# Performance work log

Measured on AMD Instinct MI355X. Metric: run time of the kernel, lower is better.

The kernel has to match this reference:

```python
import jax, jax.numpy as jnp
import numpy as np

CROP_H, CROP_W = 7, 7

def _sample_coords(lo, hi, extent, n):
    # TF crop_and_resize: coord = lo*(extent-1) + i*(hi-lo)*(extent-1)/(n-1)
    step = (hi - lo) * (extent - 1) / (n - 1)          # [N]
    return lo[:, None] * (extent - 1) + jnp.arange(n, dtype=lo.dtype)[None, :] * step[:, None]  # [N, n]

def crop_and_resize(image, boxes, box_ind, crop_h, crop_w):
    # image: [B,H,W,C], boxes: [N,4] normalized (y1,x1,y2,x2), box_ind: [N]
    B, H, W, C = image.shape
    y1, x1, y2, x2 = boxes[:, 0], boxes[:, 1], boxes[:, 2], boxes[:, 3]
    ys = _sample_coords(y1, y2, H, crop_h)             # [N, crop_h]
    xs = _sample_coords(x1, x2, W, crop_w)             # [N, crop_w]

    y0 = jnp.floor(ys); x0 = jnp.floor(xs)
    wy = (ys - y0)[:, :, None, None]                    # [N,ch,1,1] lerp weight
    wx = (xs - x0)[:, None, :, None]                    # [N,1,cw,1]
    y0i = jnp.clip(y0.astype(jnp.int32), 0, H - 1)
    y1i = jnp.clip(y0i + 1, 0, H - 1)
    x0i = jnp.clip(x0.astype(jnp.int32), 0, W - 1)
    x1i = jnp.clip(x0i + 1, 0, W - 1)

    b = box_ind[:, None, None]                          # [N,1,1]
    def corner(yi, xi):                                 # -> [N,ch,cw,C]
        return image[b, yi[:, :, None], xi[:, None, :]]

    top = corner(y0i, x0i) + (corner(y0i, x1i) - corner(y0i, x0i)) * wx
    bot = corner(y1i, x0i) + (corner(y1i, x1i) - corner(y1i, x0i)) * wx
    out = top + (bot - top) * wy                        # [N,ch,cw,C]

    # TF uses extrapolation_value=0 for samples outside the image
    vy = ((ys >= 0) & (ys <= H - 1))[:, :, None, None]
    vx = ((xs >= 0) & (xs <= W - 1))[:, None, :, None]
    return jnp.where(vy & vx, out, jnp.zeros((), out.dtype))


def setup_inputs() -> dict:
    key = jax.random.key(0)
    k1, k2, k3 = jax.random.split(key, 3)
    feats = jax.random.normal(k1, (8, 64, 64, 256), dtype=jnp.float32)
    boxes = jax.random.uniform(k2, (4000, 4), dtype=jnp.float32)
    box_ind = jax.random.randint(k3, (4000, 1), 0, 8, dtype=jnp.int32)
    return {"feats": feats, "boxes": boxes, "box_ind": box_ind}


def reference(feats, boxes, box_ind):
    ind = box_ind.reshape(-1)
    return crop_and_resize(feats, boxes, ind, CROP_H, CROP_W)
```

## Files before the change

### kernel.cpp

```cpp
#include <hip/hip_runtime.h>


#define H 64
#define W 64
#define C 256
#define CROP_HW 49
#define NIMG 8
#define G 8

typedef float f32x4 __attribute__((ext_vector_type(4)));

__global__ __launch_bounds__(512) void bucket_kernel(
    const int* __restrict__ box_ind,
    int* __restrict__ order,
    int* __restrict__ offsets,
    int n)
{
    const int wave = threadIdx.x >> 6;
    const int lane = threadIdx.x & 63;
    __shared__ int counts[NIMG];

    int cnt = 0;
    for (int i = lane; i < n; i += 64)
        cnt += (box_ind[i] == wave);
    for (int off = 32; off; off >>= 1)
        cnt += __shfl_down(cnt, off);
    if (lane == 0) counts[wave] = cnt;
    __syncthreads();

    int start = 0;
    for (int i = 0; i < wave; ++i) start += counts[i];
    if (threadIdx.x == 0) {
        int acc = 0;
        for (int i = 0; i < NIMG; ++i) { offsets[i] = acc; acc += counts[i]; }
        offsets[NIMG] = acc;
    }

    int pos = start;
    for (int base = 0; base < n; base += 64) {
        const int i = base + lane;
        const bool m = (i < n) && (box_ind[i] == wave);
        const unsigned long long mask = __ballot(m);
        const int below = __popcll(mask & ((1ULL << lane) - 1ULL));
        if (m) order[pos + below] = i;
        pos += __popcll(mask);
    }
}

struct Cell {
    int p00, p01, p10, p11;
    float wx, wy;
    bool valid;
    int oidx;
};

__device__ __forceinline__ Cell cell_info(
    int c, const int* __restrict__ order, const f32x4* __restrict__ boxes4,
    int start)
{
    Cell k;
    const int bi = c / CROP_HW;
    const int r  = c - bi * CROP_HW;
    const int iy = r / 7;
    const int ix = r - iy * 7;
    const int b  = order[start + bi];

    const f32x4 bx = boxes4[b];

    const float stepy = (bx.z - bx.x) * 63.0f / 6.0f;
    const float stepx = (bx.w - bx.y) * 63.0f / 6.0f;
    const float ys = bx.x * 63.0f + (float)iy * stepy;
    const float xs = bx.y * 63.0f + (float)ix * stepx;

    const float y0f = floorf(ys);
    const float x0f = floorf(xs);
    k.wy = ys - y0f;
    k.wx = xs - x0f;

    const int y0 = min(max((int)y0f, 0), H - 1);
    const int y1 = min(y0 + 1, H - 1);
    const int x0 = min(max((int)x0f, 0), W - 1);
    const int x1 = min(x0 + 1, W - 1);

    k.valid = (ys >= 0.0f) && (ys <= (float)(H - 1)) &&
              (xs >= 0.0f) && (xs <= (float)(W - 1));

    k.p00 = y0 * W + x0;
    k.p01 = y0 * W + x1;
    k.p10 = y1 * W + x0;
    k.p11 = y1 * W + x1;

    k.oidx = (b * CROP_HW + r) * (C / 4);
    return k;
}

__global__ __launch_bounds__(256) void crop_resize_xcd(
    const float* __restrict__ feats,
    const float* __restrict__ boxes,
    const int*   __restrict__ order,
    const int*   __restrict__ offsets,
    float*       __restrict__ out)
{
    const int img  = blockIdx.x & 7;
    const int slot = blockIdx.x >> 3;
    const int lane = threadIdx.x & 63;
    const int wv   = threadIdx.x >> 6;

    const int start   = offsets[img];
    const int nb      = offsets[img + 1] - start;
    const int ncells  = nb * CROP_HW;
    const int ngroups = (ncells + G - 1) / G;
    const int wave_local = slot * 4 + wv;
    const int stride     = (gridDim.x >> 3) * 4;

    const f32x4* __restrict__ f4 = reinterpret_cast<const f32x4*>(feats)
                                   + (size_t)img * (H * W * (C / 4));
    const f32x4* __restrict__ boxes4 = reinterpret_cast<const f32x4*>(boxes);
    f32x4* __restrict__ o4 = reinterpret_cast<f32x4*>(out);

    for (int gi = wave_local; gi < ngroups; gi += stride) {
        const int cbase = gi * G;
        const int nval  = min(G, ncells - cbase);

        int c = cbase + (lane & (G - 1));
        if (c > ncells - 1) c = ncells - 1;
        const Cell k = cell_info(c, order, boxes4, start);
        const unsigned long long vmask = __ballot(k.valid);

        #pragma unroll
        for (int j = 0; j < G; ++j) {
            if (j >= nval) break;
            const int   s00 = __builtin_amdgcn_readlane(k.p00, j);
            const int   s01 = __builtin_amdgcn_readlane(k.p01, j);
            const int   s10 = __builtin_amdgcn_readlane(k.p10, j);
            const int   s11 = __builtin_amdgcn_readlane(k.p11, j);
            const float swx = __uint_as_float(
                __builtin_amdgcn_readlane(__float_as_uint(k.wx), j));
            const float swy = __uint_as_float(
                __builtin_amdgcn_readlane(__float_as_uint(k.wy), j));
            const int   sox = __builtin_amdgcn_readlane(k.oidx, j);
            const bool  sval = (vmask >> j) & 1ULL;

            const f32x4 v00 = f4[s00 * (C / 4) + lane];
            const f32x4 v01 = f4[s01 * (C / 4) + lane];
            const f32x4 v10 = f4[s10 * (C / 4) + lane];
            const f32x4 v11 = f4[s11 * (C / 4) + lane];

            const float w11 = swx * swy;
            const float w01 = swx - w11;
            const float w10 = swy - w11;
            const float w00 = 1.0f - swx - swy + w11;

            f32x4 res = v00 * w00;
            res += v01 * w01;
            res += v10 * w10;
            res += v11 * w11;
            if (!sval) res = (f32x4)0.0f;

            __builtin_nontemporal_store(res, &o4[(size_t)sox + lane]);
        }
    }
}

extern "C" void kernel_launch(void* const* d_in, const int* in_sizes, int n_in,
                              void* d_out, int out_size, void* d_ws, size_t ws_size,
                              hipStream_t stream) {
    const float* feats   = (const float*)d_in[0];
    const float* boxes   = (const float*)d_in[1];
    const int*   box_ind = (const int*)d_in[2];
    float*       out     = (float*)d_out;

    const int n_boxes = in_sizes[1] / 4;

    int* order   = (int*)d_ws;
    int* offsets = order + n_boxes;

    bucket_kernel<<<1, 512, 0, stream>>>(box_ind, order, offsets, n_boxes);

    crop_resize_xcd<<<6144, 256, 0, stream>>>(feats, boxes, order, offsets, out);
}
```

Measured before the change: 69.74 us.

## Fuse box bucketing into crop kernel using per-block LDS ordering

Drops the separate single-block bucketing launch. Each crop block now scans box_ind itself, four waves in parallel, and builds the box list for its image in shared memory, then reads box indices from LDS. The aim is to remove the serial pre-pass and the kernel-launch dependency. The cost is that every block redundantly reads box_ind twice, and the 16KB of LDS per block can limit occupancy. The old two-kernel path is kept as a fallback when the box count exceeds 4096.

```diff
diff --git a/kernel.cpp b/kernel.cpp
--- a/kernel.cpp
+++ b/kernel.cpp
@@ -7,45 +7,9 @@
 #define CROP_HW 49
 #define NIMG 8
 #define G 8
+#define MAXB 4096
 
 typedef float f32x4 __attribute__((ext_vector_type(4)));
-
-__global__ __launch_bounds__(512) void bucket_kernel(
-    const int* __restrict__ box_ind,
-    int* __restrict__ order,
-    int* __restrict__ offsets,
-    int n)
-{
-    const int wave = threadIdx.x >> 6;
-    const int lane = threadIdx.x & 63;
-    __shared__ int counts[NIMG];
-
-    int cnt = 0;
-    for (int i = lane; i < n; i += 64)
-        cnt += (box_ind[i] == wave);
-    for (int off = 32; off; off >>= 1)
-        cnt += __shfl_down(cnt, off);
-    if (lane == 0) counts[wave] = cnt;
-    __syncthreads();
-
-    int start = 0;
-    for (int i = 0; i < wave; ++i) start += counts[i];
-    if (threadIdx.x == 0) {
-        int acc = 0;
-        for (int i = 0; i < NIMG; ++i) { offsets[i] = acc; acc += counts[i]; }
-        offsets[NIMG] = acc;
-    }
-
-    int pos = start;
-    for (int base = 0; base < n; base += 64) {
-        const int i = base + lane;
-        const bool m = (i < n) && (box_ind[i] == wave);
-        const unsigned long long mask = __ballot(m);
-        const int below = __popcll(mask & ((1ULL << lane) - 1ULL));
-        if (m) order[pos + below] = i;
-        pos += __popcll(mask);
-    }
-}
 
 struct Cell {
     int p00, p01, p10, p11;
@@ -55,15 +19,14 @@
 };
 
 __device__ __forceinline__ Cell cell_info(
-    int c, const int* __restrict__ order, const f32x4* __restrict__ boxes4,
-    int start)
+    int c, const int* order, const f32x4* __restrict__ boxes4)
 {
     Cell k;
     const int bi = c / CROP_HW;
     const int r  = c - bi * CROP_HW;
     const int iy = r / 7;
     const int ix = r - iy * 7;
-    const int b  = order[start + bi];
+    const int b  = order[bi];
 
     const f32x4 bx = boxes4[b];
 
@@ -94,20 +57,65 @@
     return k;
 }
 
+__device__ __forceinline__ int block_bucket4(
+    const int* __restrict__ box_ind, int nbox, int img, int lane, int wv,
+    int* s_order, int* s_cnt)
+{
+    const int Q  = (nbox + 3) >> 2;
+    const int lo = wv * Q;
+    const int hi = min(nbox, lo + Q);
+
+    int cnt = 0;
+    for (int base = lo; base < hi; base += 256) {
+        int a0 = (base       + lane < hi) ? box_ind[base       + lane] : -1;
+        int a1 = (base + 64  + lane < hi) ? box_ind[base + 64  + lane] : -1;
+        int a2 = (base + 128 + lane < hi) ? box_ind[base + 128 + lane] : -1;
+        int a3 = (base + 192 + lane < hi) ? box_ind[base + 192 + lane] : -1;
+        cnt += (a0 == img) + (a1 == img) + (a2 == img) + (a3 == img);
+    }
+    for (int off = 32; off; off >>= 1) cnt += __shfl_down(cnt, off);
+    if (lane == 0) s_cnt[wv] = cnt;
+    __syncthreads();
+
+    int pos = 0;
+    for (int u = 0; u < wv; ++u) pos += s_cnt[u];
+    const int nb = s_cnt[0] + s_cnt[1] + s_cnt[2] + s_cnt[3];
+
+    for (int base = lo; base < hi; base += 256) {
+        int a0 = (base       + lane < hi) ? box_ind[base       + lane] : -1;
+        int a1 = (base + 64  + lane < hi) ? box_ind[base + 64  + lane] : -1;
+        int a2 = (base + 128 + lane < hi) ? box_ind[base + 128 + lane] : -1;
+        int a3 = (base + 192 + lane < hi) ? box_ind[base + 192 + lane] : -1;
+
+        #define ROUND(A, OFF) { \
+            const bool m = (A == img); \
+            const unsigned long long mask = __ballot(m); \
+            const int below = __popcll(mask & ((1ULL << lane) - 1ULL)); \
+            if (m) s_order[pos + below] = base + OFF + lane; \
+            pos += __popcll(mask); }
+        ROUND(a0, 0) ROUND(a1, 64) ROUND(a2, 128) ROUND(a3, 192)
+        #undef ROUND
+    }
+    __syncthreads();
+    return nb;
+}
+
 __global__ __launch_bounds__(256) void crop_resize_xcd(
     const float* __restrict__ feats,
     const float* __restrict__ boxes,
-    const int*   __restrict__ order,
-    const int*   __restrict__ offsets,
-    float*       __restrict__ out)
+    const int*   __restrict__ box_ind,
+    float*       __restrict__ out,
+    int nbox)
 {
     const int img  = blockIdx.x & 7;
     const int slot = blockIdx.x >> 3;
     const int lane = threadIdx.x & 63;
     const int wv   = threadIdx.x >> 6;
 
-    const int start   = offsets[img];
-    const int nb      = offsets[img + 1] - start;
+    __shared__ int s_order[MAXB];
+    __shared__ int s_cnt[4];
+    const int nb = block_bucket4(box_ind, nbox, img, lane, wv, s_order, s_cnt);
+
     const int ncells  = nb * CROP_HW;
     const int ngroups = (ncells + G - 1) / G;
     const int wave_local = slot * 4 + wv;
@@ -124,7 +132,7 @@
 
         int c = cbase + (lane & (G - 1));
         if (c > ncells - 1) c = ncells - 1;
-        const Cell k = cell_info(c, order, boxes4, start);
+        const Cell k = cell_info(c, s_order, boxes4);
         const unsigned long long vmask = __ballot(k.valid);
 
         #pragma unroll
@@ -162,6 +170,96 @@
     }
 }
 
+__global__ __launch_bounds__(512) void bucket_kernel(
+    const int* __restrict__ box_ind, int* __restrict__ order,
+    int* __restrict__ offsets, int n)
+{
+    const int wave = threadIdx.x >> 6;
+    const int lane = threadIdx.x & 63;
+    __shared__ int counts[NIMG];
+    int cnt = 0;
+    for (int i = lane; i < n; i += 64) cnt += (box_ind[i] == wave);
+    for (int off = 32; off; off >>= 1) cnt += __shfl_down(cnt, off);
+    if (lane == 0) counts[wave] = cnt;
+    __syncthreads();
+    int start = 0;
+    for (int i = 0; i < wave; ++i) start += counts[i];
+    if (threadIdx.x == 0) {
+        int acc = 0;
+        for (int i = 0; i < NIMG; ++i) { offsets[i] = acc; acc += counts[i]; }
+        offsets[NIMG] = acc;
+    }
+    int pos = start;
+    for (int base = 0; base < n; base += 64) {
+        const int i = base + lane;
+        const bool m = (i < n) && (box_ind[i] == wave);
+        const unsigned long long mask = __ballot(m);
+        const int below = __popcll(mask & ((1ULL << lane) - 1ULL));
+        if (m) order[pos + below] = i;
+        pos += __popcll(mask);
+    }
+}
+
+__global__ __launch_bounds__(256) void crop_global_order(
+    const float* __restrict__ feats,
+    const float* __restrict__ boxes,
+    const int*   __restrict__ order,
+    const int*   __restrict__ offsets,
+    float*       __restrict__ out)
+{
+    const int img  = blockIdx.x & 7;
+    const int slot = blockIdx.x >> 3;
+    const int lane = threadIdx.x & 63;
+    const int wv   = threadIdx.x >> 6;
+    const int start   = offsets[img];
+    const int nb      = offsets[img + 1] - start;
+    const int ncells  = nb * CROP_HW;
+    const int ngroups = (ncells + G - 1) / G;
+    const int wave_local = slot * 4 + wv;
+    const int stride     = (gridDim.x >> 3) * 4;
+    const f32x4* __restrict__ f4 = reinterpret_cast<const f32x4*>(feats)
+                                   + (size_t)img * (H * W * (C / 4));
+    const f32x4* __restrict__ boxes4 = reinterpret_cast<const f32x4*>(boxes);
+    f32x4* __restrict__ o4 = reinterpret_cast<f32x4*>(out);
+
+    for (int gi = wave_local; gi < ngroups; gi += stride) {
+        const int cbase = gi * G;
+        const int nval  = min(G, ncells - cbase);
+        int c = cbase + (lane & (G - 1));
+        if (c > ncells - 1) c = ncells - 1;
+        const Cell k = cell_info(c, order + start, boxes4);
+        const unsigned long long vmask = __ballot(k.valid);
+        #pragma unroll
+        for (int j = 0; j < G; ++j) {
+            if (j >= nval) break;
+            const int   s00 = __builtin_amdgcn_readlane(k.p00, j);
+            const int   s01 = __builtin_amdgcn_readlane(k.p01, j);
+            const int   s10 = __builtin_amdgcn_readlane(k.p10, j);
+            const int   s11 = __builtin_amdgcn_readlane(k.p11, j);
+            const float swx = __uint_as_float(
+                __builtin_amdgcn_readlane(__float_as_uint(k.wx), j));
+            const float swy = __uint_as_float(
+                __builtin_amdgcn_readlane(__float_as_uint(k.wy), j));
+            const int   sox = __builtin_amdgcn_readlane(k.oidx, j);
+            const bool  sval = (vmask >> j) & 1ULL;
+            const f32x4 v00 = f4[s00 * (C / 4) + lane];
+            const f32x4 v01 = f4[s01 * (C / 4) + lane];
+            const f32x4 v10 = f4[s10 * (C / 4) + lane];
+            const f32x4 v11 = f4[s11 * (C / 4) + lane];
+            const float w11 = swx * swy;
+            const float w01 = swx - w11;
+            const float w10 = swy - w11;
+            const float w00 = 1.0f - swx - swy + w11;
+            f32x4 res = v00 * w00;
+            res += v01 * w01;
+            res += v10 * w10;
+            res += v11 * w11;
+            if (!sval) res = (f32x4)0.0f;
+            __builtin_nontemporal_store(res, &o4[(size_t)sox + lane]);
+        }
+    }
+}
+
 extern "C" void kernel_launch(void* const* d_in, const int* in_sizes, int n_in,
                               void* d_out, int out_size, void* d_ws, size_t ws_size,
                               hipStream_t stream) {
@@ -172,10 +270,14 @@
 
     const int n_boxes = in_sizes[1] / 4;
 
-    int* order   = (int*)d_ws;
-    int* offsets = order + n_boxes;
-
-    bucket_kernel<<<1, 512, 0, stream>>>(box_ind, order, offsets, n_boxes);
-
-    crop_resize_xcd<<<6144, 256, 0, stream>>>(feats, boxes, order, offsets, out);
-}
+    if (n_boxes <= MAXB) {
+        crop_resize_xcd<<<6144, 256, 0, stream>>>(feats, boxes, box_ind, out,
+                                                  n_boxes);
+    } else {
+        int* order   = (int*)d_ws;
+        int* offsets = order + n_boxes;
+        bucket_kernel<<<1, 512, 0, stream>>>(box_ind, order, offsets, n_boxes);
+        crop_global_order<<<6144, 256, 0, stream>>>(feats, boxes, order,
+                                                    offsets, out);
+    }
+}
```

New measurement: 60.70 us, median of 5. -13.0%, faster.
